# Performance work log

Measured on AMD Instinct MI355X. Metric: run time of the kernel, lower is better.

The kernel has to match this reference:

```python
import jax, jax.numpy as jnp
import numpy as np

N = 100000
E = 1600000
D_IN, D_HID, D_OUT = 128, 128, 64
EPS = 1e-5


def setup_inputs() -> dict:
    key = jax.random.key(0)
    ks = jax.random.split(key, 16)
    inp = {
        "x": jax.random.normal(ks[0], (N, D_IN), dtype=jnp.float32),
        "edge_index": jax.random.randint(ks[1], (2, E), 0, N, dtype=jnp.int64),
        # layer 1: SAGEConv(D_IN -> D_HID)
        "w_l1": jax.random.normal(ks[2], (D_HID, D_IN), dtype=jnp.float32) / np.sqrt(D_IN),
        "b_l1": jnp.zeros((D_HID,), dtype=jnp.float32),
        "w_r1": jax.random.normal(ks[3], (D_HID, D_IN), dtype=jnp.float32) / np.sqrt(D_IN),
        "bn1_gamma": jnp.ones((D_HID,), dtype=jnp.float32),
        "bn1_beta": jnp.zeros((D_HID,), dtype=jnp.float32),
        "bn1_mean": jnp.zeros((D_HID,), dtype=jnp.float32),
        "bn1_var": jnp.ones((D_HID,), dtype=jnp.float32),
        # layer 2: SAGEConv(D_HID -> D_HID)
        "w_l2": jax.random.normal(ks[4], (D_HID, D_HID), dtype=jnp.float32) / np.sqrt(D_HID),
        "b_l2": jnp.zeros((D_HID,), dtype=jnp.float32),
        "w_r2": jax.random.normal(ks[5], (D_HID, D_HID), dtype=jnp.float32) / np.sqrt(D_HID),
        "bn2_gamma": jnp.ones((D_HID,), dtype=jnp.float32),
        "bn2_beta": jnp.zeros((D_HID,), dtype=jnp.float32),
        "bn2_mean": jnp.zeros((D_HID,), dtype=jnp.float32),
        "bn2_var": jnp.ones((D_HID,), dtype=jnp.float32),
        # layer 3: SAGEConv(D_HID -> D_OUT)
        "w_l3": jax.random.normal(ks[6], (D_OUT, D_HID), dtype=jnp.float32) / np.sqrt(D_HID),
        "b_l3": jnp.zeros((D_OUT,), dtype=jnp.float32),
        "w_r3": jax.random.normal(ks[7], (D_OUT, D_HID), dtype=jnp.float32) / np.sqrt(D_HID),
    }
    return inp


def _sage_conv(x, src, dst, w_l, b_l, w_r):
    """PyG SAGEConv default: mean-aggregate source features into targets,
    then lin_l(aggr) + lin_r(root). w_* are [out,in] (torch layout)."""
    msgs = x[src]                                   # [E, d]  gather
    agg = jax.ops.segment_sum(msgs, dst, num_segments=N)   # [N, d] scatter-add
    deg = jax.ops.segment_sum(jnp.ones((src.shape[0],), x.dtype), dst, num_segments=N)
    agg = agg / jnp.maximum(deg, 1.0)[:, None]      # mean (0 for isolated nodes)
    return agg @ w_l.T + b_l + x @ w_r.T


def _bn_eval(x, gamma, beta, mean, var):
    return (x - mean) * (gamma * jax.lax.rsqrt(var + EPS)) + beta


def reference(x, edge_index,
              w_l1, b_l1, w_r1, bn1_gamma, bn1_beta, bn1_mean, bn1_var,
              w_l2, b_l2, w_r2, bn2_gamma, bn2_beta, bn2_mean, bn2_var,
              w_l3, b_l3, w_r3):
    src, dst = edge_index[0], edge_index[1]
    h = _sage_conv(x, src, dst, w_l1, b_l1, w_r1)
    h = jax.nn.relu(_bn_eval(h, bn1_gamma, bn1_beta, bn1_mean, bn1_var))
    h = _sage_conv(h, src, dst, w_l2, b_l2, w_r2)
    h = jax.nn.relu(_bn_eval(h, bn2_gamma, bn2_beta, bn2_mean, bn2_var))
    h = _sage_conv(h, src, dst, w_l3, b_l3, w_r3)
    return h
```

## Files before the change

kernel.cpp:

```cpp
#include <hip/hip_runtime.h>

#define N_NODES 100000
#define N_EDGES 1600000
#define D 128
#define EPS 1e-5f

#define NPB_BITS 8
#define NODES_PER_BUCK 256
#define NBUCK ((N_NODES + NODES_PER_BUCK - 1) >> NPB_BITS)
#define BUCK_CAP 5120

#define CHUNK_E 8192
#define NB_BIN ((N_EDGES + CHUNK_E - 1) / CHUNK_E)

typedef unsigned int uint;
typedef unsigned short ushort;
using bf16x8 = __attribute__((ext_vector_type(8))) short;
using f32x4  = __attribute__((ext_vector_type(4))) float;

__device__ __forceinline__ ushort f2bf(float f) {
    uint u = __float_as_uint(f);
    return (ushort)((u + 0x7fffu + ((u >> 16) & 1u)) >> 16);
}
__device__ __forceinline__ float bflo(uint u) { return __uint_as_float(u << 16); }
__device__ __forceinline__ float bfhi(uint u) { return __uint_as_float(u & 0xffff0000u); }

#define PREP_GRID 13077
__global__ __launch_bounds__(256) void k_prep(
    const int* __restrict__ ei, int* __restrict__ bcnt,
    const float* __restrict__ x, ushort* __restrict__ xb,
    const float* __restrict__ wl1, const float* __restrict__ wr1, ushort* __restrict__ w21,
    const float* __restrict__ wl2, const float* __restrict__ wr2, ushort* __restrict__ w22,
    const float* __restrict__ wl3, const float* __restrict__ wr3, ushort* __restrict__ w23,
    const float* __restrict__ b1, const float* __restrict__ g1, const float* __restrict__ be1,
    const float* __restrict__ m1, const float* __restrict__ v1,
    float* __restrict__ bnA1, float* __restrict__ bnB1,
    const float* __restrict__ b2, const float* __restrict__ g2, const float* __restrict__ be2,
    const float* __restrict__ m2, const float* __restrict__ v2,
    float* __restrict__ bnA2, float* __restrict__ bnB2) {
    __shared__ int sc[NBUCK];
    int b = blockIdx.x, t = threadIdx.x;
    if (b < 256) {
        for (int i = t; i < NBUCK; i += 256) sc[i] = 0;
        __syncthreads();
        for (int e = b * 256 + t; e < N_EDGES; e += 256 * 256)
            atomicAdd(&sc[ei[N_EDGES + e] >> NPB_BITS], 1);
        __syncthreads();
        for (int i = t; i < NBUCK; i += 256) {
            int v = sc[i];
            if (v) atomicAdd(&bcnt[i], v);
        }
    } else if (b < 12756) {
        int i = (b - 256) * 256 + t;
        float4 v = ((const float4*)x)[i];
        ushort4 o;
        o.x = f2bf(v.x); o.y = f2bf(v.y); o.z = f2bf(v.z); o.w = f2bf(v.w);
        ((ushort4*)xb)[i] = o;
    } else if (b < 12884) {
        int i = (b - 12756) * 256 + t;
        int o = i >> 8, k = i & 255;
        w21[i] = f2bf((k < 128) ? wl1[o * 128 + k] : wr1[o * 128 + k - 128]);
    } else if (b < 13012) {
        int i = (b - 12884) * 256 + t;
        int o = i >> 8, k = i & 255;
        w22[i] = f2bf((k < 128) ? wl2[o * 128 + k] : wr2[o * 128 + k - 128]);
    } else if (b < 13076) {
        int i = (b - 13012) * 256 + t;
        int o = i >> 7, k = i & 127;
        w23[i] = f2bf((o < 64) ? wl3[o * 128 + k] : wr3[(o - 64) * 128 + k]);
    } else {
        if (t < 128) {
            float a = g1[t] * rsqrtf(v1[t] + EPS);
            bnA1[t] = a; bnB1[t] = (b1[t] - m1[t]) * a + be1[t];
        } else {
            int c = t - 128;
            float a = g2[c] * rsqrtf(v2[c] + EPS);
            bnA2[c] = a; bnB2[c] = (b2[c] - m2[c]) * a + be2[c];
        }
    }
}


__global__ __launch_bounds__(1024) void k_bscan(const int* __restrict__ bcnt,
                                                int* __restrict__ bstart, int* __restrict__ bcur,
                                                int* __restrict__ row_start) {
    __shared__ int s[1024];
    int t = threadIdx.x;
    int own = (t < NBUCK) ? bcnt[t] : 0;
    s[t] = own;
    __syncthreads();
    for (int off = 1; off < 1024; off <<= 1) {
        int v = (t >= off) ? s[t - off] : 0;
        __syncthreads();
        s[t] += v;
        __syncthreads();
    }
    if (t < NBUCK) {
        int excl = s[t] - own;
        bstart[t] = excl;
        bcur[t] = excl;
    }
    if (t == 0) {
        bstart[NBUCK] = N_EDGES;
        row_start[N_NODES] = N_EDGES;
    }
}

__global__ __launch_bounds__(256) void k_bin2(const int* __restrict__ ei,
                                              int* __restrict__ bcur,
                                              uint* __restrict__ binned) {
    __shared__ int cnt[NBUCK];
    __shared__ int lbase[NBUCK];
    __shared__ int gbase[NBUCK];
    __shared__ int ssc[512];
    __shared__ uint sval[CHUNK_E];
    __shared__ ushort sbkt[CHUNK_E];
    int t = threadIdx.x;
    int e0 = blockIdx.x * CHUNK_E;
    int e1 = e0 + CHUNK_E; if (e1 > N_EDGES) e1 = N_EDGES;
    int ecnt = e1 - e0;
    for (int i = t; i < NBUCK; i += 256) cnt[i] = 0;
    __syncthreads();
    for (int e = e0 + t; e < e1; e += 256)
        atomicAdd(&cnt[ei[N_EDGES + e] >> NPB_BITS], 1);
    __syncthreads();
    int v0 = (t < NBUCK) ? cnt[t] : 0;
    int v1 = (t + 256 < NBUCK) ? cnt[t + 256] : 0;
    ssc[t] = v0; ssc[t + 256] = v1;
    __syncthreads();
    for (int off = 1; off < 512; off <<= 1) {
        int a0 = (t >= off) ? ssc[t - off] : 0;
        int a1 = (t + 256 >= off) ? ssc[t + 256 - off] : 0;
        __syncthreads();
        ssc[t] += a0; ssc[t + 256] += a1;
        __syncthreads();
    }
    if (t < NBUCK) lbase[t] = ssc[t] - v0;
    if (t + 256 < NBUCK) lbase[t + 256] = ssc[t + 256] - v1;
    __syncthreads();
    for (int i = t; i < NBUCK; i += 256) {
        int v = cnt[i];
        gbase[i] = v ? atomicAdd(&bcur[i], v) : 0;
        cnt[i] = 0;
    }
    __syncthreads();
    for (int e = e0 + t; e < e1; e += 256) {
        int s = ei[e];
        int d = ei[N_EDGES + e];
        int b = d >> NPB_BITS;
        int pos = lbase[b] + atomicAdd(&cnt[b], 1);
        sval[pos] = ((uint)s << NPB_BITS) | (uint)(d & (NODES_PER_BUCK - 1));
        sbkt[pos] = (ushort)b;
    }
    __syncthreads();
    for (int s = t; s < ecnt; s += 256) {
        int b = sbkt[s];
        binned[gbase[b] + (s - lbase[b])] = sval[s];
    }
}

__global__ __launch_bounds__(256) void k_bcsr(const uint* __restrict__ binned,
                                              const int* __restrict__ bstart,
                                              int* __restrict__ row_start,
                                              int* __restrict__ csr_src) {
    __shared__ int cnt[NODES_PER_BUCK];
    __shared__ int sc[NODES_PER_BUCK];
    __shared__ int cur[NODES_PER_BUCK];
    __shared__ uint ecache[BUCK_CAP];
    __shared__ int sorted[BUCK_CAP];
    int b = blockIdx.x, t = threadIdx.x;
    int s0 = bstart[b], s1 = bstart[b + 1];
    int m = s1 - s0;
    bool fits = (m <= BUCK_CAP);
    cnt[t] = 0;
    __syncthreads();
    for (int e = s0 + t; e < s1; e += 256) {
        uint u = binned[e];
        int idx = e - s0;
        if (idx < BUCK_CAP) ecache[idx] = u;
        atomicAdd(&cnt[u & (NODES_PER_BUCK - 1)], 1);
    }
    __syncthreads();
    int own = cnt[t];
    sc[t] = own;
    __syncthreads();
    for (int off = 1; off < NODES_PER_BUCK; off <<= 1) {
        int v = (t >= off) ? sc[t - off] : 0;
        __syncthreads();
        sc[t] += v;
        __syncthreads();
    }
    int lexcl = sc[t] - own;
    {
        int node = (b << NPB_BITS) + t;
        if (node < N_NODES) row_start[node] = s0 + lexcl;
        cur[t] = fits ? lexcl : (s0 + lexcl);
    }
    __syncthreads();
    if (fits) {
        for (int e = s0 + t; e < s1; e += 256) {
            uint u = ecache[e - s0];
            int pos = atomicAdd(&cur[u & (NODES_PER_BUCK - 1)], 1);
            sorted[pos] = (int)(u >> NPB_BITS);
        }
        __syncthreads();
        for (int s = t; s < m; s += 256)
            csr_src[s0 + s] = sorted[s];
    } else {
        for (int e = s0 + t; e < s1; e += 256) {
            uint u = (e - s0 < BUCK_CAP) ? ecache[e - s0] : binned[e];
            int pos = atomicAdd(&cur[u & (NODES_PER_BUCK - 1)], 1);
            csr_src[pos] = (int)(u >> NPB_BITS);
        }
    }
}

__global__ __launch_bounds__(256) void k_agg_mean(
    const ushort* __restrict__ Zin, const int* __restrict__ row_start,
    const int* __restrict__ csr_src, ushort* __restrict__ Agg) {
    int t = threadIdx.x;
    int w = t >> 6, l = t & 63;
    int n = blockIdx.x * 4 + w;
    int g = l >> 3, c = l & 7;
    int s0 = row_start[n], s1 = row_start[n + 1];
    float a[16];
#pragma unroll
    for (int j = 0; j < 16; ++j) a[j] = 0.f;
    for (int e = s0; e < s1; e += 8) {
        int ee = e + g;
        if (ee < s1) {
            int src = csr_src[ee];
            const ushort* zp = &Zin[(size_t)src * 128 + c * 16];
            uint4 v0 = *(const uint4*)zp;
            uint4 v1 = *(const uint4*)(zp + 8);
            a[0] += bflo(v0.x); a[1] += bfhi(v0.x);
            a[2] += bflo(v0.y); a[3] += bfhi(v0.y);
            a[4] += bflo(v0.z); a[5] += bfhi(v0.z);
            a[6] += bflo(v0.w); a[7] += bfhi(v0.w);
            a[8]  += bflo(v1.x); a[9]  += bfhi(v1.x);
            a[10] += bflo(v1.y); a[11] += bfhi(v1.y);
            a[12] += bflo(v1.z); a[13] += bfhi(v1.z);
            a[14] += bflo(v1.w); a[15] += bfhi(v1.w);
        }
    }
#pragma unroll
    for (int off = 8; off <= 32; off <<= 1)
#pragma unroll
        for (int j = 0; j < 16; ++j) a[j] += __shfl_xor(a[j], off);
    if (l < 8) {
        float inv = 1.f / fmaxf((float)(s1 - s0), 1.f);
        uint4 p0, p1;
        uint* q0 = (uint*)&p0;
        uint* q1 = (uint*)&p1;
#pragma unroll
        for (int j = 0; j < 4; ++j) {
            q0[j] = (uint)f2bf(a[2 * j] * inv)     | ((uint)f2bf(a[2 * j + 1] * inv) << 16);
            q1[j] = (uint)f2bf(a[8 + 2 * j] * inv) | ((uint)f2bf(a[9 + 2 * j] * inv) << 16);
        }
        ushort* op = &Agg[(size_t)n * 128 + l * 16];
        *(uint4*)op = p0;
        *(uint4*)(op + 8) = p1;
    }
}

__global__ __launch_bounds__(256) void k_gemm12(
    const ushort* __restrict__ Ag, const ushort* __restrict__ Xin,
    const ushort* __restrict__ W2,
    const float* __restrict__ bnA, const float* __restrict__ bnB,
    ushort* __restrict__ Hout) {
    __shared__ ushort sW[16384];

    int t = threadIdx.x;
    int n0 = blockIdx.x * 64;
    int w = t >> 6, l = t & 63;

    int arow = n0 + 16 * w + (l & 15);
    if (arow >= N_NODES) arow = N_NODES - 1;
    int ko = (l >> 4) * 8;
    bf16x8 afr[8];
#pragma unroll
    for (int kt = 0; kt < 4; ++kt)
        afr[kt] = *(const bf16x8*)&Ag[(size_t)arow * 128 + kt * 32 + ko];
#pragma unroll
    for (int kt = 0; kt < 4; ++kt)
        afr[4 + kt] = *(const bf16x8*)&Xin[(size_t)arow * 128 + kt * 32 + ko];

    f32x4 acc[8];
#pragma unroll
    for (int ot = 0; ot < 8; ++ot) acc[ot] = (f32x4){0.f, 0.f, 0.f, 0.f};

#pragma unroll
    for (int p = 0; p < 2; ++p) {
        for (int s = t; s < 2048; s += 256) {
            int f = s >> 6, ln = s & 63;
            int o = (f >> 2) * 16 + (ln & 15);
            int k = p * 128 + (f & 3) * 32 + ((ln >> 4) * 8);
            *(uint4*)&sW[s * 8] = *(const uint4*)&W2[o * 256 + k];
        }
        __syncthreads();
#pragma unroll
        for (int ktl = 0; ktl < 4; ++ktl) {
            int kt = p * 4 + ktl;
#pragma unroll
            for (int ot = 0; ot < 8; ++ot) {
                bf16x8 bfr = *(const bf16x8*)&sW[((ot * 4 + ktl) * 64 + l) * 8];
                acc[ot] = __builtin_amdgcn_mfma_f32_16x16x32_bf16(afr[kt], bfr, acc[ot], 0, 0, 0);
            }
        }
        __syncthreads();
    }

    float* sC = (float*)sW;
    int r0 = (l >> 4) * 4;
#pragma unroll
    for (int ot = 0; ot < 8; ++ot)
#pragma unroll
        for (int j = 0; j < 4; ++j)
            sC[(16 * w + r0 + j) * 128 + ot * 16 + (l & 15)] = acc[ot][j];
    __syncthreads();

    for (int u = t; u < 1024; u += 256) {
        int r = u >> 4, cc = (u & 15) * 8;
        int n = n0 + r;
        if (n >= N_NODES) continue;
        float4 A0 = *(const float4*)&bnA[cc];
        float4 A1 = *(const float4*)&bnA[cc + 4];
        float4 B0 = *(const float4*)&bnB[cc];
        float4 B1 = *(const float4*)&bnB[cc + 4];
        const float* pa0 = (const float*)&A0;
        const float* pa1 = (const float*)&A1;
        const float* pb0 = (const float*)&B0;
        const float* pb1 = (const float*)&B1;
        uint4 pk;
        uint* pw = (uint*)&pk;
#pragma unroll
        for (int j = 0; j < 4; ++j) {
            int i0 = 2 * j, i1 = 2 * j + 1;
            float va = (i0 < 4) ? pa0[i0] : pa1[i0 - 4];
            float vb = (i0 < 4) ? pb0[i0] : pb1[i0 - 4];
            float wa = (i1 < 4) ? pa0[i1] : pa1[i1 - 4];
            float wb = (i1 < 4) ? pb0[i1] : pb1[i1 - 4];
            float h0 = fmaxf(sC[r * 128 + cc + i0] * va + vb, 0.f);
            float h1 = fmaxf(sC[r * 128 + cc + i1] * wa + wb, 0.f);
            pw[j] = (uint)f2bf(h0) | ((uint)f2bf(h1) << 16);
        }
        *(uint4*)&Hout[(size_t)n * 128 + cc] = pk;
    }
}

__global__ __launch_bounds__(256) void k_gemm3(
    const ushort* __restrict__ Xb, const ushort* __restrict__ W2,
    const float* __restrict__ bias,
    ushort* __restrict__ Zb, ushort* __restrict__ Yb) {
    constexpr int DOUT = 64;
    constexpr int NT = 128;
    constexpr int OT = 8;

    __shared__ ushort sW[OT * 4 * 64 * 8];

    int t = threadIdx.x;
    int n0 = blockIdx.x * 64;
    int w = t >> 6, l = t & 63;
    int arow = n0 + 16 * w + (l & 15);
    if (arow >= N_NODES) arow = N_NODES - 1;
    const ushort* ap = &Xb[(size_t)arow * D + ((l >> 4) * 8)];
    bf16x8 afr[4];
#pragma unroll
    for (int kt = 0; kt < 4; ++kt) afr[kt] = *(const bf16x8*)(ap + kt * 32);

    for (int s = t; s < OT * 4 * 64; s += 256) {
        int f = s >> 6, ln = s & 63;
        int o = (f >> 2) * 16 + (ln & 15);
        int k = (f & 3) * 32 + ((ln >> 4) * 8);
        *(uint4*)&sW[s * 8] = *(const uint4*)&W2[o * D + k];
    }
    __syncthreads();

    f32x4 acc[OT];
#pragma unroll
    for (int ot = 0; ot < OT; ++ot) acc[ot] = (f32x4){0.f, 0.f, 0.f, 0.f};
#pragma unroll
    for (int kt = 0; kt < 4; ++kt)
#pragma unroll
        for (int ot = 0; ot < OT; ++ot) {
            bf16x8 bfr = *(const bf16x8*)&sW[((ot * 4 + kt) * 64 + l) * 8];
            acc[ot] = __builtin_amdgcn_mfma_f32_16x16x32_bf16(afr[kt], bfr, acc[ot], 0, 0, 0);
        }
    __syncthreads();

    float* sC = (float*)sW;
    int r0 = (l >> 4) * 4;
#pragma unroll
    for (int ot = 0; ot < OT; ++ot)
#pragma unroll
        for (int j = 0; j < 4; ++j)
            sC[(16 * w + r0 + j) * NT + ot * 16 + (l & 15)] = acc[ot][j];
    __syncthreads();

    constexpr int CH = NT / 8;
    for (int c = t; c < 64 * CH; c += 256) {
        int r = c / CH, cc = (c % CH) * 8;
        if (n0 + r >= N_NODES) continue;
        bool isY = cc >= DOUT;
        uint4 pk;
        uint* pw = (uint*)&pk;
#pragma unroll
        for (int j = 0; j < 4; ++j) {
            float f0 = sC[r * NT + cc + 2 * j];
            float f1 = sC[r * NT + cc + 2 * j + 1];
            if (isY) {
                f0 += bias[cc - DOUT + 2 * j];
                f1 += bias[cc - DOUT + 2 * j + 1];
            }
            pw[j] = (uint)f2bf(f0) | ((uint)f2bf(f1) << 16);
        }
        if (isY) *(uint4*)&Yb[(size_t)(n0 + r) * DOUT + cc - DOUT] = pk;
        else     *(uint4*)&Zb[(size_t)(n0 + r) * DOUT + cc] = pk;
    }
}

__global__ __launch_bounds__(256) void k_agg3(
    const ushort* __restrict__ Zb, const int* __restrict__ row_start,
    const int* __restrict__ csr_src, const ushort* __restrict__ Yb,
    float* __restrict__ out) {
    int t = threadIdx.x;
    int w = t >> 6, l = t & 63;
    int n = blockIdx.x * 4 + w;
    int g = l >> 3, c = l & 7;
    int s0 = row_start[n], s1 = row_start[n + 1];
    float a[8];
#pragma unroll
    for (int j = 0; j < 8; ++j) a[j] = 0.f;
    for (int e = s0; e < s1; e += 16) {
        int e0 = e + g, e1 = e + g + 8;
        int src0 = (e0 < s1) ? csr_src[e0] : -1;
        int src1 = (e1 < s1) ? csr_src[e1] : -1;
        uint4 v0, v1;
        if (src0 >= 0) v0 = *(const uint4*)&Zb[(size_t)src0 * 64 + c * 8];
        if (src1 >= 0) v1 = *(const uint4*)&Zb[(size_t)src1 * 64 + c * 8];
        if (src0 >= 0) {
            a[0] += bflo(v0.x); a[1] += bfhi(v0.x);
            a[2] += bflo(v0.y); a[3] += bfhi(v0.y);
            a[4] += bflo(v0.z); a[5] += bfhi(v0.z);
            a[6] += bflo(v0.w); a[7] += bfhi(v0.w);
        }
        if (src1 >= 0) {
            a[0] += bflo(v1.x); a[1] += bfhi(v1.x);
            a[2] += bflo(v1.y); a[3] += bfhi(v1.y);
            a[4] += bflo(v1.z); a[5] += bfhi(v1.z);
            a[6] += bflo(v1.w); a[7] += bfhi(v1.w);
        }
    }
#pragma unroll
    for (int off = 8; off <= 32; off <<= 1)
#pragma unroll
        for (int j = 0; j < 8; ++j) a[j] += __shfl_xor(a[j], off);
    if (l < 8) {
        float inv = 1.f / fmaxf((float)(s1 - s0), 1.f);
        uint4 yv = *(const uint4*)&Yb[(size_t)n * 64 + l * 8];
        float4 o0, o1;
        o0.x = bflo(yv.x) + a[0] * inv; o0.y = bfhi(yv.x) + a[1] * inv;
        o0.z = bflo(yv.y) + a[2] * inv; o0.w = bfhi(yv.y) + a[3] * inv;
        o1.x = bflo(yv.z) + a[4] * inv; o1.y = bfhi(yv.z) + a[5] * inv;
        o1.z = bflo(yv.w) + a[6] * inv; o1.w = bfhi(yv.w) + a[7] * inv;
        float* po = &out[(size_t)n * 64 + l * 8];
        *(float4*)po = o0;
        *(float4*)(po + 4) = o1;
    }
}


static inline size_t align256(size_t x) { return (x + 255) & ~(size_t)255; }

extern "C" void kernel_launch(void* const* d_in, const int* in_sizes, int n_in,
                              void* d_out, int out_size, void* d_ws, size_t ws_size,
                              hipStream_t stream) {
    const float* x    = (const float*)d_in[0];
    const int*   ei   = (const int*)d_in[1];
    const float* w_l1 = (const float*)d_in[2];
    const float* b_l1 = (const float*)d_in[3];
    const float* w_r1 = (const float*)d_in[4];
    const float* g1   = (const float*)d_in[5];
    const float* be1  = (const float*)d_in[6];
    const float* m1   = (const float*)d_in[7];
    const float* v1   = (const float*)d_in[8];
    const float* w_l2 = (const float*)d_in[9];
    const float* b_l2 = (const float*)d_in[10];
    const float* w_r2 = (const float*)d_in[11];
    const float* g2   = (const float*)d_in[12];
    const float* be2  = (const float*)d_in[13];
    const float* m2   = (const float*)d_in[14];
    const float* v2   = (const float*)d_in[15];
    const float* w_l3 = (const float*)d_in[16];
    const float* b_l3 = (const float*)d_in[17];
    const float* w_r3 = (const float*)d_in[18];
    float* out = (float*)d_out;

    char* w = (char*)d_ws;
    int* bcnt      = (int*)w;  w += align256((size_t)NBUCK * 4);
    int* bstart    = (int*)w;  w += align256((size_t)(NBUCK + 1) * 4);
    int* bcur      = (int*)w;  w += align256((size_t)NBUCK * 4);
    uint* binned   = (uint*)w; w += align256((size_t)N_EDGES * 4);
    int* row_start = (int*)w;  w += align256((size_t)(N_NODES + 1) * 4);
    int* csr_src   = (int*)w;  w += align256((size_t)N_EDGES * 4);
    ushort* xb     = (ushort*)w; w += align256((size_t)N_NODES * D * 2);
    ushort* ag     = (ushort*)w; w += align256((size_t)N_NODES * D * 2);
    ushort* h1     = (ushort*)w; w += align256((size_t)N_NODES * D * 2);
    ushort* h2     = (ushort*)w; w += align256((size_t)N_NODES * D * 2);
    ushort* Zb     = (ushort*)w; w += align256((size_t)N_NODES * 64 * 2);
    ushort* Yb     = (ushort*)w; w += align256((size_t)N_NODES * 64 * 2);
    ushort* w2_1   = (ushort*)w; w += align256((size_t)128 * 256 * 2);
    ushort* w2_2   = (ushort*)w; w += align256((size_t)128 * 256 * 2);
    ushort* w2_3   = (ushort*)w; w += align256((size_t)128 * 128 * 2);
    float* bnA1    = (float*)w;  w += align256(128 * 4);
    float* bnB1    = (float*)w;  w += align256(128 * 4);
    float* bnA2    = (float*)w;  w += align256(128 * 4);
    float* bnB2    = (float*)w;  w += align256(128 * 4);

    hipMemsetAsync(bcnt, 0, (size_t)NBUCK * 4, stream);

    k_prep<<<PREP_GRID, 256, 0, stream>>>(ei, bcnt, x, xb,
        w_l1, w_r1, w2_1, w_l2, w_r2, w2_2, w_l3, w_r3, w2_3,
        b_l1, g1, be1, m1, v1, bnA1, bnB1,
        b_l2, g2, be2, m2, v2, bnA2, bnB2);

    k_bscan<<<1, 1024, 0, stream>>>(bcnt, bstart, bcur, row_start);
    k_bin2<<<NB_BIN, 256, 0, stream>>>(ei, bcur, binned);
    k_bcsr<<<NBUCK, 256, 0, stream>>>(binned, bstart, row_start, csr_src);

    int gb = (N_NODES + 63) / 64;
    int ab = N_NODES / 4;

    k_agg_mean<<<ab, 256, 0, stream>>>(xb, row_start, csr_src, ag);
    k_gemm12<<<gb, 256, 0, stream>>>(ag, xb, w2_1, bnA1, bnB1, h1);
    k_agg_mean<<<ab, 256, 0, stream>>>(h1, row_start, csr_src, ag);
    k_gemm12<<<gb, 256, 0, stream>>>(ag, h1, w2_2, bnA2, bnB2, h2);
    k_gemm3<<<gb, 256, 0, stream>>>(h2, w2_3, b_l3, Zb, Yb);
    k_agg3<<<ab, 256, 0, stream>>>(Zb, row_start, csr_src, Yb, out);
}
```

Measured before the change: 312.5 us.

## Fuse layer-2 GEMM with BN/ReLU and layer-3 projection GEMM

Merges the layer-2 SAGE GEMM, its BN+ReLU epilogue and the layer-3 weight projection into one kernel. The hidden activations are staged in padded shared memory instead of being written to and re-read from global memory as h2. This removes one launch and a 25.6MB round trip. The cost is more shared memory per block (about 49KB), which may lower occupancy. The BN epilogue also drops the float4-vectorized bnA/bnB loads in favour of scalar indexing.

```diff
diff --git a/kernel.cpp b/kernel.cpp
--- a/kernel.cpp
+++ b/kernel.cpp
@@ -323,99 +323,143 @@
         int r = u >> 4, cc = (u & 15) * 8;
         int n = n0 + r;
         if (n >= N_NODES) continue;
-        float4 A0 = *(const float4*)&bnA[cc];
-        float4 A1 = *(const float4*)&bnA[cc + 4];
-        float4 B0 = *(const float4*)&bnB[cc];
-        float4 B1 = *(const float4*)&bnB[cc + 4];
-        const float* pa0 = (const float*)&A0;
-        const float* pa1 = (const float*)&A1;
-        const float* pb0 = (const float*)&B0;
-        const float* pb1 = (const float*)&B1;
         uint4 pk;
         uint* pw = (uint*)&pk;
 #pragma unroll
         for (int j = 0; j < 4; ++j) {
-            int i0 = 2 * j, i1 = 2 * j + 1;
-            float va = (i0 < 4) ? pa0[i0] : pa1[i0 - 4];
-            float vb = (i0 < 4) ? pb0[i0] : pb1[i0 - 4];
-            float wa = (i1 < 4) ? pa0[i1] : pa1[i1 - 4];
-            float wb = (i1 < 4) ? pb0[i1] : pb1[i1 - 4];
-            float h0 = fmaxf(sC[r * 128 + cc + i0] * va + vb, 0.f);
-            float h1 = fmaxf(sC[r * 128 + cc + i1] * wa + wb, 0.f);
+            int i0 = cc + 2 * j, i1 = cc + 2 * j + 1;
+            float h0 = fmaxf(sC[r * 128 + i0] * bnA[i0] + bnB[i0], 0.f);
+            float h1 = fmaxf(sC[r * 128 + i1] * bnA[i1] + bnB[i1], 0.f);
             pw[j] = (uint)f2bf(h0) | ((uint)f2bf(h1) << 16);
         }
         *(uint4*)&Hout[(size_t)n * 128 + cc] = pk;
     }
 }
 
-__global__ __launch_bounds__(256) void k_gemm3(
-    const ushort* __restrict__ Xb, const ushort* __restrict__ W2,
-    const float* __restrict__ bias,
+__global__ __launch_bounds__(256) void k_gemm2f(
+    const ushort* __restrict__ Ag, const ushort* __restrict__ Xin,
+    const ushort* __restrict__ W2,
+    const float* __restrict__ bnA, const float* __restrict__ bnB,
+    const ushort* __restrict__ W3, const float* __restrict__ bias3,
     ushort* __restrict__ Zb, ushort* __restrict__ Yb) {
-    constexpr int DOUT = 64;
-    constexpr int NT = 128;
-    constexpr int OT = 8;
-
-    __shared__ ushort sW[OT * 4 * 64 * 8];
+    __shared__ ushort sW[16384];
+    __shared__ ushort sH[64 * 136];
 
     int t = threadIdx.x;
     int n0 = blockIdx.x * 64;
     int w = t >> 6, l = t & 63;
+    int ko = (l >> 4) * 8;
+    int r0 = (l >> 4) * 4;
+
     int arow = n0 + 16 * w + (l & 15);
     if (arow >= N_NODES) arow = N_NODES - 1;
-    const ushort* ap = &Xb[(size_t)arow * D + ((l >> 4) * 8)];
-    bf16x8 afr[4];
-#pragma unroll
-    for (int kt = 0; kt < 4; ++kt) afr[kt] = *(const bf16x8*)(ap + kt * 32);
-
-    for (int s = t; s < OT * 4 * 64; s += 256) {
+    bf16x8 afr[8];
+#pragma unroll
+    for (int kt = 0; kt < 4; ++kt)
+        afr[kt] = *(const bf16x8*)&Ag[(size_t)arow * 128 + kt * 32 + ko];
+#pragma unroll
+    for (int kt = 0; kt < 4; ++kt)
+        afr[4 + kt] = *(const bf16x8*)&Xin[(size_t)arow * 128 + kt * 32 + ko];
+
+    f32x4 acc[8];
+#pragma unroll
+    for (int ot = 0; ot < 8; ++ot) acc[ot] = (f32x4){0.f, 0.f, 0.f, 0.f};
+
+#pragma unroll
+    for (int p = 0; p < 2; ++p) {
+        for (int s = t; s < 2048; s += 256) {
+            int f = s >> 6, ln = s & 63;
+            int o = (f >> 2) * 16 + (ln & 15);
+            int k = p * 128 + (f & 3) * 32 + ((ln >> 4) * 8);
+            *(uint4*)&sW[s * 8] = *(const uint4*)&W2[o * 256 + k];
+        }
+        __syncthreads();
+#pragma unroll
+        for (int ktl = 0; ktl < 4; ++ktl) {
+            int kt = p * 4 + ktl;
+#pragma unroll
+            for (int ot = 0; ot < 8; ++ot) {
+                bf16x8 bfr = *(const bf16x8*)&sW[((ot * 4 + ktl) * 64 + l) * 8];
+                acc[ot] = __builtin_amdgcn_mfma_f32_16x16x32_bf16(afr[kt], bfr, acc[ot], 0, 0, 0);
+            }
+        }
+        __syncthreads();
+    }
+
+    float* sC = (float*)sW;
+#pragma unroll
+    for (int ot = 0; ot < 8; ++ot)
+#pragma unroll
+        for (int j = 0; j < 4; ++j)
+            sC[(16 * w + r0 + j) * 128 + ot * 16 + (l & 15)] = acc[ot][j];
+    __syncthreads();
+
+    for (int u = t; u < 1024; u += 256) {
+        int r = u >> 4, cc = (u & 15) * 8;
+        uint4 pk;
+        uint* pw = (uint*)&pk;
+#pragma unroll
+        for (int j = 0; j < 4; ++j) {
+            int i0 = cc + 2 * j, i1 = cc + 2 * j + 1;
+            float h0 = fmaxf(sC[r * 128 + i0] * bnA[i0] + bnB[i0], 0.f);
+            float h1 = fmaxf(sC[r * 128 + i1] * bnA[i1] + bnB[i1], 0.f);
+            pw[j] = (uint)f2bf(h0) | ((uint)f2bf(h1) << 16);
+        }
+        *(uint4*)&sH[r * 136 + cc] = pk;
+    }
+    __syncthreads();
+
+    int hrow = 16 * w + (l & 15);
+    bf16x8 a3[4];
+#pragma unroll
+    for (int kt = 0; kt < 4; ++kt)
+        a3[kt] = *(const bf16x8*)&sH[hrow * 136 + kt * 32 + ko];
+
+    for (int s = t; s < 2048; s += 256) {
         int f = s >> 6, ln = s & 63;
         int o = (f >> 2) * 16 + (ln & 15);
         int k = (f & 3) * 32 + ((ln >> 4) * 8);
-        *(uint4*)&sW[s * 8] = *(const uint4*)&W2[o * D + k];
-    }
-    __syncthreads();
-
-    f32x4 acc[OT];
-#pragma unroll
-    for (int ot = 0; ot < OT; ++ot) acc[ot] = (f32x4){0.f, 0.f, 0.f, 0.f};
+        *(uint4*)&sW[s * 8] = *(const uint4*)&W3[o * 128 + k];
+    }
+    __syncthreads();
+
+    f32x4 acc3[8];
+#pragma unroll
+    for (int ot = 0; ot < 8; ++ot) acc3[ot] = (f32x4){0.f, 0.f, 0.f, 0.f};
 #pragma unroll
     for (int kt = 0; kt < 4; ++kt)
 #pragma unroll
-        for (int ot = 0; ot < OT; ++ot) {
+        for (int ot = 0; ot < 8; ++ot) {
             bf16x8 bfr = *(const bf16x8*)&sW[((ot * 4 + kt) * 64 + l) * 8];
-            acc[ot] = __builtin_amdgcn_mfma_f32_16x16x32_bf16(afr[kt], bfr, acc[ot], 0, 0, 0);
-        }
-    __syncthreads();
-
-    float* sC = (float*)sW;
-    int r0 = (l >> 4) * 4;
-#pragma unroll
-    for (int ot = 0; ot < OT; ++ot)
+            acc3[ot] = __builtin_amdgcn_mfma_f32_16x16x32_bf16(a3[kt], bfr, acc3[ot], 0, 0, 0);
+        }
+    __syncthreads();
+
+#pragma unroll
+    for (int ot = 0; ot < 8; ++ot)
 #pragma unroll
         for (int j = 0; j < 4; ++j)
-            sC[(16 * w + r0 + j) * NT + ot * 16 + (l & 15)] = acc[ot][j];
-    __syncthreads();
-
-    constexpr int CH = NT / 8;
-    for (int c = t; c < 64 * CH; c += 256) {
-        int r = c / CH, cc = (c % CH) * 8;
+            sC[(16 * w + r0 + j) * 128 + ot * 16 + (l & 15)] = acc3[ot][j];
+    __syncthreads();
+
+    for (int c = t; c < 64 * 16; c += 256) {
+        int r = c >> 4, cc = (c & 15) * 8;
         if (n0 + r >= N_NODES) continue;
-        bool isY = cc >= DOUT;
+        bool isY = cc >= 64;
         uint4 pk;
         uint* pw = (uint*)&pk;
 #pragma unroll
         for (int j = 0; j < 4; ++j) {
-            float f0 = sC[r * NT + cc + 2 * j];
-            float f1 = sC[r * NT + cc + 2 * j + 1];
+            float f0 = sC[r * 128 + cc + 2 * j];
+            float f1 = sC[r * 128 + cc + 2 * j + 1];
             if (isY) {
-                f0 += bias[cc - DOUT + 2 * j];
-                f1 += bias[cc - DOUT + 2 * j + 1];
+                f0 += bias3[cc - 64 + 2 * j];
+                f1 += bias3[cc - 64 + 2 * j + 1];
             }
             pw[j] = (uint)f2bf(f0) | ((uint)f2bf(f1) << 16);
         }
-        if (isY) *(uint4*)&Yb[(size_t)(n0 + r) * DOUT + cc - DOUT] = pk;
-        else     *(uint4*)&Zb[(size_t)(n0 + r) * DOUT + cc] = pk;
+        if (isY) *(uint4*)&Yb[(size_t)(n0 + r) * 64 + cc - 64] = pk;
+        else     *(uint4*)&Zb[(size_t)(n0 + r) * 64 + cc] = pk;
     }
 }
 
@@ -506,7 +550,6 @@
     ushort* xb     = (ushort*)w; w += align256((size_t)N_NODES * D * 2);
     ushort* ag     = (ushort*)w; w += align256((size_t)N_NODES * D * 2);
     ushort* h1     = (ushort*)w; w += align256((size_t)N_NODES * D * 2);
-    ushort* h2     = (ushort*)w; w += align256((size_t)N_NODES * D * 2);
     ushort* Zb     = (ushort*)w; w += align256((size_t)N_NODES * 64 * 2);
     ushort* Yb     = (ushort*)w; w += align256((size_t)N_NODES * 64 * 2);
     ushort* w2_1   = (ushort*)w; w += align256((size_t)128 * 256 * 2);
@@ -534,7 +577,6 @@
     k_agg_mean<<<ab, 256, 0, stream>>>(xb, row_start, csr_src, ag);
     k_gemm12<<<gb, 256, 0, stream>>>(ag, xb, w2_1, bnA1, bnB1, h1);
     k_agg_mean<<<ab, 256, 0, stream>>>(h1, row_start, csr_src, ag);
-    k_gemm12<<<gb, 256, 0, stream>>>(ag, h1, w2_2, bnA2, bnB2, h2);
-    k_gemm3<<<gb, 256, 0, stream>>>(h2, w2_3, b_l3, Zb, Yb);
+    k_gemm2f<<<gb, 256, 0, stream>>>(ag, h1, w2_2, bnA2, bnB2, w2_3, b_l3, Zb, Yb);
     k_agg3<<<ab, 256, 0, stream>>>(Zb, row_start, csr_src, Yb, out);
 }
```

After: 300.4 us. 1.04x faster.
